# Performance work log

Measured on AMD Instinct MI355X. Metric: run time of the kernel, lower is better.

## Reference

```python
import jax, jax.numpy as jnp
import numpy as np

WINDOW_SIZE = 11
SIGMA = 1.5
LEVELS = 5
WEIGHTS = np.array([0.0448, 0.2856, 0.3001, 0.2363, 0.1333], dtype=np.float32)
C1 = 0.01 ** 2  # (0.01 * L)^2, L = 1
C2 = 0.03 ** 2


def _gauss_window(channel):
    x = np.arange(WINDOW_SIZE, dtype=np.float32) - WINDOW_SIZE // 2
    g = np.exp(-x ** 2 / (2.0 * SIGMA ** 2)).astype(np.float32)
    g = g / g.sum()
    w2 = np.outer(g, g)  # [ws, ws]
    w = np.broadcast_to(w2, (channel, 1, WINDOW_SIZE, WINDOW_SIZE)).copy()
    return jnp.asarray(w)


def _dwconv(x, w, channel):
    # depthwise conv, padding=0 (VALID), groups=channel
    return jax.lax.conv_general_dilated(
        x, w, window_strides=(1, 1), padding='VALID',
        dimension_numbers=('NCHW', 'OIHW', 'NCHW'),
        feature_group_count=channel)


def _ssim(img1, img2, window, channel):
    mu1 = _dwconv(img1, window, channel)
    mu2 = _dwconv(img2, window, channel)
    mu1_sq = mu1 * mu1
    mu2_sq = mu2 * mu2
    mu1_mu2 = mu1 * mu2
    sigma1_sq = _dwconv(img1 * img1, window, channel) - mu1_sq
    sigma2_sq = _dwconv(img2 * img2, window, channel) - mu2_sq
    sigma12 = _dwconv(img1 * img2, window, channel) - mu1_mu2
    v1 = 2.0 * sigma12 + C2
    v2 = sigma1_sq + sigma2_sq + C2
    cs = jnp.mean(v1 / v2)
    ssim_map = (2.0 * mu1_mu2 + C1) * v1 / ((mu1_sq + mu2_sq + C1) * v2)
    return jnp.mean(ssim_map), cs


def _avg_pool2(x):
    # avg_pool2d(kernel=2, stride=2), VALID
    s = jax.lax.reduce_window(x, 0.0, jax.lax.add, (1, 1, 2, 2), (1, 1, 2, 2), 'VALID')
    return s * 0.25


def setup_inputs() -> dict:
    key = jax.random.key(0)
    k1, k2 = jax.random.split(key)
    img1 = jax.random.uniform(k1, (16, 3, 512, 512), dtype=jnp.float32)
    img2 = jax.random.uniform(k2, (16, 3, 512, 512), dtype=jnp.float32)
    return {"img1": img1, "img2": img2}


def reference(img1, img2):
    channel = img1.shape[1]
    window = _gauss_window(channel)
    weights = jnp.asarray(WEIGHTS)
    mssim, mcs = [], []
    a, b = img1, img2
    for _ in range(LEVELS):  # fixed pyramid depth, shapes differ per level
        s, c = _ssim(a, b, window, channel)
        mssim.append(s)
        mcs.append(c)
        a = _avg_pool2(a)
        b = _avg_pool2(b)
    mssim = (jnp.stack(mssim) + 1.0) * 0.5  # normalize=True
    mcs = (jnp.stack(mcs) + 1.0) * 0.5
    return jnp.prod(mcs[:-1] ** weights[:-1]) * mssim[-1] ** weights[-1]
```

## Files before the change

### kernel.cpp

```cpp
#include <hip/hip_runtime.h>
#include <math.h>

#define WS 11
#define PAD 10
#define TW 32
#define TH 32
#define IH 42
#define NC 48
#define C1V 1.0e-4f
#define C2V 9.0e-4f

struct Params { float g[WS]; };
struct ROff { int off[5]; int cnt[5]; float inv[5]; };

template<int POOL>
__global__ __launch_bounds__(256, 6) void ssim_level_kernel(
    const float* __restrict__ img1, const float* __restrict__ img2,
    float* __restrict__ pool1, float* __restrict__ pool2,
    int H, int OH, int tilesX, Params P,
    float2* __restrict__ partial, int partial_off)
{
    __shared__ float4 rp[IH][TW];
    __shared__ float reds[4], redc[4];

    const int tid   = threadIdx.x;
    const int tileX = blockIdx.x % tilesX;
    const int tileY = blockIdx.x / tilesX;
    const int img   = blockIdx.y;
    const size_t ib = (size_t)img * H * H;
    const float* __restrict__ p1 = img1 + ib;
    const float* __restrict__ p2 = img2 + ib;
    const int ox0 = tileX * TW;
    const int oy0 = tileY * TH;

    for (int u = tid; u < IH * 8; u += 256) {
        const int r = u >> 3, cg = u & 7;
        const int y = min(oy0 + r, H - 1);
        const float* __restrict__ rowa = p1 + (size_t)y * H;
        const float* __restrict__ rowb = p2 + (size_t)y * H;
        float sv[16], dv[16];
#pragma unroll
        for (int q = 0; q < 4; ++q) {
            const int x = min(ox0 + cg * 4 + q * 4, H - 4);
            const float4 va = *(const float4*)(rowa + x);
            const float4 vb = *(const float4*)(rowb + x);
            sv[q*4+0] = va.x + vb.x;  dv[q*4+0] = va.x - vb.x;
            sv[q*4+1] = va.y + vb.y;  dv[q*4+1] = va.y - vb.y;
            sv[q*4+2] = va.z + vb.z;  dv[q*4+2] = va.z - vb.z;
            sv[q*4+3] = va.w + vb.w;  dv[q*4+3] = va.w - vb.w;
        }
        float m0[4] = {0,0,0,0}, m1[4] = {0,0,0,0};
        float m2[4] = {0,0,0,0}, m3[4] = {0,0,0,0};
#pragma unroll
        for (int i = 0; i < 14; ++i) {
            const float s = sv[i], d = dv[i];
            const float ss = s * s, dd = d * d;
#pragma unroll
            for (int j = 0; j < 4; ++j) {
                const int k = i - j;
                if (k >= 0 && k < WS) {
                    const float g = P.g[k];
                    m0[j] += g * s;  m1[j] += g * d;
                    m2[j] += g * ss; m3[j] += g * dd;
                }
            }
        }
        const int c0 = cg * 4, sw = r & 7;
#pragma unroll
        for (int j = 0; j < 4; ++j)
            rp[r][(c0 + j) ^ sw] = make_float4(m0[j], m1[j], m2[j], m3[j]);
    }
    __syncthreads();

    const int c  = tid & 31;
    const int r0 = (tid >> 5) * 4;
    float A0[4]={0,0,0,0}, A1[4]={0,0,0,0}, A2[4]={0,0,0,0}, A3[4]={0,0,0,0};
#pragma unroll
    for (int k = 0; k < 14; ++k) {
        const int R = r0 + k;
        const float4 v = rp[R][c ^ (R & 7)];
#pragma unroll
        for (int j = 0; j < 4; ++j) {
            const int t = k - j;
            if (t >= 0 && t < WS) {
                const float g = P.g[t];
                A0[j] += g * v.x; A1[j] += g * v.y;
                A2[j] += g * v.z; A3[j] += g * v.w;
            }
        }
    }
    float ssim_acc = 0.f, cs_acc = 0.f;
    const int ox = ox0 + c;
#pragma unroll
    for (int j = 0; j < 4; ++j) {
        const int oy = oy0 + r0 + j;
        if (oy < OH && ox < OH) {
            const float ms = A0[j], md = A1[j], Es = A2[j], Ed = A3[j];
            const float ms2 = ms * ms, md2 = md * md;
            const float mu12 = 0.25f * (ms2 - md2);
            const float musq = 0.5f  * (ms2 + md2);
            const float v1 = 0.5f * (Es - Ed) - 2.f * mu12 + C2V;
            const float v2 = 0.5f * (Es + Ed) - musq + C2V;
            const float rv2 = __builtin_amdgcn_rcpf(v2);
            const float cs  = v1 * rv2;
            const float ssim = (2.f * mu12 + C1V) *
                               __builtin_amdgcn_rcpf(musq + C1V) * cs;
            ssim_acc += ssim;
            cs_acc   += cs;
        }
    }

    if (POOL) {
        const int px = tid & 15, py = tid >> 4;
        const int yy = oy0 + 2 * py;
        const int xx = ox0 + 2 * px;
        const float2 a0 = *(const float2*)(p1 + (size_t)yy * H + xx);
        const float2 a1 = *(const float2*)(p1 + (size_t)(yy + 1) * H + xx);
        const float2 b0 = *(const float2*)(p2 + (size_t)yy * H + xx);
        const float2 b1 = *(const float2*)(p2 + (size_t)(yy + 1) * H + xx);
        const int h = H >> 1;
        const size_t ob = (size_t)img * h * h + (size_t)((oy0 >> 1) + py) * h + (ox0 >> 1) + px;
        pool1[ob] = 0.25f * (a0.x + a0.y + a1.x + a1.y);
        pool2[ob] = 0.25f * (b0.x + b0.y + b1.x + b1.y);
    }

#pragma unroll
    for (int off = 32; off > 0; off >>= 1) {
        ssim_acc += __shfl_down(ssim_acc, off);
        cs_acc   += __shfl_down(cs_acc, off);
    }
    const int wave = tid >> 6, lane = tid & 63;
    if (lane == 0) { reds[wave] = ssim_acc; redc[wave] = cs_acc; }
    __syncthreads();
    if (tid == 0) {
        const float s  = reds[0] + reds[1] + reds[2] + reds[3];
        const float cc = redc[0] + redc[1] + redc[2] + redc[3];
        partial[(size_t)partial_off + (size_t)blockIdx.y * gridDim.x + blockIdx.x] =
            make_float2(s, cc);
    }
}

__global__ __launch_bounds__(256) void reduce_final_kernel(
    const float2* __restrict__ partial, ROff ro, float* __restrict__ out)
{
    __shared__ float sS[5], sC[5];
    __shared__ float reds[4], redc[4];
    const int tid = threadIdx.x;
    for (int l = 0; l < 5; ++l) {
        float s = 0.f, c = 0.f;
        for (int i = tid; i < ro.cnt[l]; i += 256) {
            const float2 v = partial[ro.off[l] + i];
            s += v.x; c += v.y;
        }
#pragma unroll
        for (int off = 32; off > 0; off >>= 1) {
            s += __shfl_down(s, off);
            c += __shfl_down(c, off);
        }
        const int wave = tid >> 6, lane = tid & 63;
        if (lane == 0) { reds[wave] = s; redc[wave] = c; }
        __syncthreads();
        if (tid == 0) {
            sS[l] = (reds[0] + reds[1] + reds[2] + reds[3]) * ro.inv[l];
            sC[l] = (redc[0] + redc[1] + redc[2] + redc[3]) * ro.inv[l];
        }
        __syncthreads();
    }
    if (tid == 0) {
        const float w[5] = {0.0448f, 0.2856f, 0.3001f, 0.2363f, 0.1333f};
        float prod = 1.f;
#pragma unroll
        for (int i = 0; i < 4; ++i)
            prod *= powf((sC[i] + 1.f) * 0.5f, w[i]);
        prod *= powf((sS[4] + 1.f) * 0.5f, w[4]);
        out[0] = prod;
    }
}

extern "C" void kernel_launch(void* const* d_in, const int* in_sizes, int n_in,
                              void* d_out, int out_size, void* d_ws, size_t ws_size,
                              hipStream_t stream)
{
    const float* img1 = (const float*)d_in[0];
    const float* img2 = (const float*)d_in[1];
    float* out = (float*)d_out;
    float* ws  = (float*)d_ws;

    Params P;
    {
        double g[WS], sum = 0.0;
        for (int i = 0; i < WS; ++i) {
            double x = (double)i - (WS / 2);
            g[i] = exp(-x * x / (2.0 * 1.5 * 1.5));
            sum += g[i];
        }
        for (int i = 0; i < WS; ++i) P.g[i] = (float)(g[i] / sum);
    }

    float* p1[5]; float* p2[5];
    p1[0] = (float*)img1; p2[0] = (float*)img2;
    size_t o = 0;
    for (int l = 1; l < 5; ++l) {
        const int H = 512 >> l;
        p1[l] = ws + o; o += (size_t)NC * H * H;
        p2[l] = ws + o; o += (size_t)NC * H * H;
    }
    float2* partial = (float2*)(ws + o);
    (void)ws_size; (void)in_sizes; (void)n_in; (void)out_size;

    ROff ro;
    {
        int off = 0;
        for (int l = 0; l < 5; ++l) {
            const int H = 512 >> l, OH = H - PAD;
            const int tiles = (OH + TW - 1) / TW;
            ro.off[l] = off;
            ro.cnt[l] = tiles * tiles * NC;
            ro.inv[l] = 1.f / ((float)NC * OH * OH);
            off += ro.cnt[l];
        }
    }

    for (int l = 0; l < 5; ++l) {
        const int H = 512 >> l, OH = H - PAD;
        const int tiles = (OH + TW - 1) / TW;
        const dim3 grid(tiles * tiles, NC);
        if (l < 4)
            ssim_level_kernel<1><<<grid, 256, 0, stream>>>(
                p1[l], p2[l], p1[l + 1], p2[l + 1], H, OH, tiles, P, partial, ro.off[l]);
        else
            ssim_level_kernel<0><<<grid, 256, 0, stream>>>(
                p1[l], p2[l], nullptr, nullptr, H, OH, tiles, P, partial, ro.off[l]);
    }

    reduce_final_kernel<<<1, 256, 0, stream>>>(partial, ro, out);
}
```

Measured before the change: 119.7 us.

## Process vertical strips of tiles with a ring buffer to reuse halo rows

The per-tile SSIM kernel becomes a strip kernel. Each block walks CH vertically stacked 32x32 tiles and keeps the horizontal-convolution rows in a 64-row shared-memory ring buffer. The 10-row vertical halo is then computed once per strip rather than once per tile, which cuts redundant row-convolution work and global loads on the large levels. In exchange there are fewer blocks, serialized iterations with two barriers each, a lower launch-bounds occupancy hint, and an odd-stride padded layout in place of the XOR swizzle.

```diff
diff --git a/kernel.cpp b/kernel.cpp
--- a/kernel.cpp
+++ b/kernel.cpp
@@ -3,125 +3,143 @@
 
 #define WS 11
 #define PAD 10
-#define TW 32
-#define TH 32
-#define IH 42
 #define NC 48
 #define C1V 1.0e-4f
 #define C2V 9.0e-4f
+#define BROWS 64
+#define RST 33
 
 struct Params { float g[WS]; };
 struct ROff { int off[5]; int cnt[5]; float inv[5]; };
 
-template<int POOL>
-__global__ __launch_bounds__(256, 6) void ssim_level_kernel(
+__device__ __forceinline__ void row_conv_unit(
+    const float* __restrict__ rowa, const float* __restrict__ rowb,
+    const int xq[4], int cg, float4* __restrict__ rprow, const Params& P)
+{
+    float sv[16], dv[16];
+#pragma unroll
+    for (int q = 0; q < 4; ++q) {
+        const float4 va = *(const float4*)(rowa + xq[q]);
+        const float4 vb = *(const float4*)(rowb + xq[q]);
+        sv[q*4+0]=va.x+vb.x; dv[q*4+0]=va.x-vb.x;
+        sv[q*4+1]=va.y+vb.y; dv[q*4+1]=va.y-vb.y;
+        sv[q*4+2]=va.z+vb.z; dv[q*4+2]=va.z-vb.z;
+        sv[q*4+3]=va.w+vb.w; dv[q*4+3]=va.w-vb.w;
+    }
+    float m0[4]={0,0,0,0}, m1[4]={0,0,0,0}, m2[4]={0,0,0,0}, m3[4]={0,0,0,0};
+#pragma unroll
+    for (int i = 0; i < 14; ++i) {
+        const float s = sv[i], d = dv[i];
+        const float ss = s*s, dd = d*d;
+#pragma unroll
+        for (int j = 0; j < 4; ++j) {
+            const int k = i - j;
+            if (k >= 0 && k < WS) {
+                const float g = P.g[k];
+                m0[j]+=g*s; m1[j]+=g*d; m2[j]+=g*ss; m3[j]+=g*dd;
+            }
+        }
+    }
+#pragma unroll
+    for (int j = 0; j < 4; ++j)
+        rprow[cg*4 + j] = make_float4(m0[j], m1[j], m2[j], m3[j]);
+}
+
+template<int CH, int POOL>
+__global__ __launch_bounds__(256, 4) void ssim_strip_kernel(
     const float* __restrict__ img1, const float* __restrict__ img2,
     float* __restrict__ pool1, float* __restrict__ pool2,
     int H, int OH, int tilesX, Params P,
     float2* __restrict__ partial, int partial_off)
 {
-    __shared__ float4 rp[IH][TW];
+    __shared__ float4 rp[BROWS][RST];
     __shared__ float reds[4], redc[4];
-
     const int tid   = threadIdx.x;
     const int tileX = blockIdx.x % tilesX;
-    const int tileY = blockIdx.x / tilesX;
+    const int ty    = blockIdx.x / tilesX;
     const int img   = blockIdx.y;
     const size_t ib = (size_t)img * H * H;
     const float* __restrict__ p1 = img1 + ib;
     const float* __restrict__ p2 = img2 + ib;
-    const int ox0 = tileX * TW;
-    const int oy0 = tileY * TH;
-
-    for (int u = tid; u < IH * 8; u += 256) {
-        const int r = u >> 3, cg = u & 7;
-        const int y = min(oy0 + r, H - 1);
-        const float* __restrict__ rowa = p1 + (size_t)y * H;
-        const float* __restrict__ rowb = p2 + (size_t)y * H;
-        float sv[16], dv[16];
-#pragma unroll
-        for (int q = 0; q < 4; ++q) {
-            const int x = min(ox0 + cg * 4 + q * 4, H - 4);
-            const float4 va = *(const float4*)(rowa + x);
-            const float4 vb = *(const float4*)(rowb + x);
-            sv[q*4+0] = va.x + vb.x;  dv[q*4+0] = va.x - vb.x;
-            sv[q*4+1] = va.y + vb.y;  dv[q*4+1] = va.y - vb.y;
-            sv[q*4+2] = va.z + vb.z;  dv[q*4+2] = va.z - vb.z;
-            sv[q*4+3] = va.w + vb.w;  dv[q*4+3] = va.w - vb.w;
-        }
-        float m0[4] = {0,0,0,0}, m1[4] = {0,0,0,0};
-        float m2[4] = {0,0,0,0}, m3[4] = {0,0,0,0};
-#pragma unroll
-        for (int i = 0; i < 14; ++i) {
-            const float s = sv[i], d = dv[i];
-            const float ss = s * s, dd = d * d;
+    const int ox0 = tileX * 32;
+    const int oy0 = ty * (CH * 32);
+
+    const int r_unit = tid >> 3;
+    const int cg     = tid & 7;
+    int xq[4];
+#pragma unroll
+    for (int q = 0; q < 4; ++q) xq[q] = min(ox0 + cg*4 + q*4, H - 4);
+
+    const int cc  = tid & 31;
+    const int r0c = (tid >> 5) * 4;
+
+    if (tid < 80) {
+        const int Y = r_unit;
+        const int y = min(oy0 + Y, H - 1);
+        row_conv_unit(p1 + (size_t)y*H, p2 + (size_t)y*H, xq, cg,
+                      &rp[Y & (BROWS-1)][0], P);
+    }
+
+    float ssim_acc = 0.f, cs_acc = 0.f;
+
+    for (int t = 0; t < CH; ++t) {
+        {
+            const int Y = t*32 + 10 + r_unit;
+            const int y = min(oy0 + Y, H - 1);
+            row_conv_unit(p1 + (size_t)y*H, p2 + (size_t)y*H, xq, cg,
+                          &rp[Y & (BROWS-1)][0], P);
+        }
+        __syncthreads();
+
+        float A0[4]={0,0,0,0}, A1[4]={0,0,0,0}, A2[4]={0,0,0,0}, A3[4]={0,0,0,0};
+#pragma unroll
+        for (int k = 0; k < 14; ++k) {
+            const int Y = t*32 + r0c + k;
+            const float4 v = rp[Y & (BROWS-1)][cc];
 #pragma unroll
             for (int j = 0; j < 4; ++j) {
-                const int k = i - j;
-                if (k >= 0 && k < WS) {
-                    const float g = P.g[k];
-                    m0[j] += g * s;  m1[j] += g * d;
-                    m2[j] += g * ss; m3[j] += g * dd;
+                const int tt = k - j;
+                if (tt >= 0 && tt < WS) {
+                    const float g = P.g[tt];
+                    A0[j]+=g*v.x; A1[j]+=g*v.y; A2[j]+=g*v.z; A3[j]+=g*v.w;
                 }
             }
         }
-        const int c0 = cg * 4, sw = r & 7;
-#pragma unroll
-        for (int j = 0; j < 4; ++j)
-            rp[r][(c0 + j) ^ sw] = make_float4(m0[j], m1[j], m2[j], m3[j]);
-    }
-    __syncthreads();
-
-    const int c  = tid & 31;
-    const int r0 = (tid >> 5) * 4;
-    float A0[4]={0,0,0,0}, A1[4]={0,0,0,0}, A2[4]={0,0,0,0}, A3[4]={0,0,0,0};
-#pragma unroll
-    for (int k = 0; k < 14; ++k) {
-        const int R = r0 + k;
-        const float4 v = rp[R][c ^ (R & 7)];
+        const int ox = ox0 + cc;
 #pragma unroll
         for (int j = 0; j < 4; ++j) {
-            const int t = k - j;
-            if (t >= 0 && t < WS) {
-                const float g = P.g[t];
-                A0[j] += g * v.x; A1[j] += g * v.y;
-                A2[j] += g * v.z; A3[j] += g * v.w;
+            const int oy = oy0 + t*32 + r0c + j;
+            if (oy < OH && ox < OH) {
+                const float ms = A0[j], md = A1[j], Es = A2[j], Ed = A3[j];
+                const float ms2 = ms*ms, md2 = md*md;
+                const float mu12 = 0.25f * (ms2 - md2);
+                const float musq = 0.5f  * (ms2 + md2);
+                const float v1 = 0.5f * (Es - Ed) - 2.f*mu12 + C2V;
+                const float v2 = 0.5f * (Es + Ed) - musq + C2V;
+                const float rv2 = __builtin_amdgcn_rcpf(v2);
+                const float cs  = v1 * rv2;
+                const float ssim = (2.f*mu12 + C1V) *
+                                   __builtin_amdgcn_rcpf(musq + C1V) * cs;
+                ssim_acc += ssim;
+                cs_acc   += cs;
             }
         }
-    }
-    float ssim_acc = 0.f, cs_acc = 0.f;
-    const int ox = ox0 + c;
-#pragma unroll
-    for (int j = 0; j < 4; ++j) {
-        const int oy = oy0 + r0 + j;
-        if (oy < OH && ox < OH) {
-            const float ms = A0[j], md = A1[j], Es = A2[j], Ed = A3[j];
-            const float ms2 = ms * ms, md2 = md * md;
-            const float mu12 = 0.25f * (ms2 - md2);
-            const float musq = 0.5f  * (ms2 + md2);
-            const float v1 = 0.5f * (Es - Ed) - 2.f * mu12 + C2V;
-            const float v2 = 0.5f * (Es + Ed) - musq + C2V;
-            const float rv2 = __builtin_amdgcn_rcpf(v2);
-            const float cs  = v1 * rv2;
-            const float ssim = (2.f * mu12 + C1V) *
-                               __builtin_amdgcn_rcpf(musq + C1V) * cs;
-            ssim_acc += ssim;
-            cs_acc   += cs;
-        }
-    }
-
-    if (POOL) {
-        const int px = tid & 15, py = tid >> 4;
-        const int yy = oy0 + 2 * py;
-        const int xx = ox0 + 2 * px;
-        const float2 a0 = *(const float2*)(p1 + (size_t)yy * H + xx);
-        const float2 a1 = *(const float2*)(p1 + (size_t)(yy + 1) * H + xx);
-        const float2 b0 = *(const float2*)(p2 + (size_t)yy * H + xx);
-        const float2 b1 = *(const float2*)(p2 + (size_t)(yy + 1) * H + xx);
-        const int h = H >> 1;
-        const size_t ob = (size_t)img * h * h + (size_t)((oy0 >> 1) + py) * h + (ox0 >> 1) + px;
-        pool1[ob] = 0.25f * (a0.x + a0.y + a1.x + a1.y);
-        pool2[ob] = 0.25f * (b0.x + b0.y + b1.x + b1.y);
+
+        if (POOL) {
+            const int px = tid & 15, py = tid >> 4;
+            const int yy = oy0 + t*32 + 2*py;
+            const int xx = ox0 + 2*px;
+            const float2 a0 = *(const float2*)(p1 + (size_t)yy*H + xx);
+            const float2 a1 = *(const float2*)(p1 + (size_t)(yy+1)*H + xx);
+            const float2 b0 = *(const float2*)(p2 + (size_t)yy*H + xx);
+            const float2 b1 = *(const float2*)(p2 + (size_t)(yy+1)*H + xx);
+            const int h = H >> 1;
+            const size_t ob = (size_t)img*h*h +
+                              (size_t)(((oy0 + t*32) >> 1) + py)*h + (ox0 >> 1) + px;
+            pool1[ob] = 0.25f * (a0.x + a0.y + a1.x + a1.y);
+            pool2[ob] = 0.25f * (b0.x + b0.y + b1.x + b1.y);
+        }
+        __syncthreads();
     }
 
 #pragma unroll
@@ -134,9 +152,9 @@
     __syncthreads();
     if (tid == 0) {
         const float s  = reds[0] + reds[1] + reds[2] + reds[3];
-        const float cc = redc[0] + redc[1] + redc[2] + redc[3];
+        const float cc2 = redc[0] + redc[1] + redc[2] + redc[3];
         partial[(size_t)partial_off + (size_t)blockIdx.y * gridDim.x + blockIdx.x] =
-            make_float2(s, cc);
+            make_float2(s, cc2);
     }
 }
 
@@ -208,14 +226,16 @@
     float2* partial = (float2*)(ws + o);
     (void)ws_size; (void)in_sizes; (void)n_in; (void)out_size;
 
+    const int CHv[5] = {4, 2, 1, 1, 1};
     ROff ro;
     {
         int off = 0;
         for (int l = 0; l < 5; ++l) {
             const int H = 512 >> l, OH = H - PAD;
-            const int tiles = (OH + TW - 1) / TW;
+            const int tilesX = (OH + 31) / 32;
+            const int tilesY = (OH + CHv[l]*32 - 1) / (CHv[l]*32);
             ro.off[l] = off;
-            ro.cnt[l] = tiles * tiles * NC;
+            ro.cnt[l] = tilesX * tilesY * NC;
             ro.inv[l] = 1.f / ((float)NC * OH * OH);
             off += ro.cnt[l];
         }
@@ -223,14 +243,31 @@
 
     for (int l = 0; l < 5; ++l) {
         const int H = 512 >> l, OH = H - PAD;
-        const int tiles = (OH + TW - 1) / TW;
-        const dim3 grid(tiles * tiles, NC);
-        if (l < 4)
-            ssim_level_kernel<1><<<grid, 256, 0, stream>>>(
-                p1[l], p2[l], p1[l + 1], p2[l + 1], H, OH, tiles, P, partial, ro.off[l]);
-        else
-            ssim_level_kernel<0><<<grid, 256, 0, stream>>>(
-                p1[l], p2[l], nullptr, nullptr, H, OH, tiles, P, partial, ro.off[l]);
+        const int tilesX = (OH + 31) / 32;
+        const int tilesY = (OH + CHv[l]*32 - 1) / (CHv[l]*32);
+        const dim3 grid(tilesX * tilesY, NC);
+        switch (l) {
+        case 0:
+            ssim_strip_kernel<4,1><<<grid, 256, 0, stream>>>(
+                p1[0], p2[0], p1[1], p2[1], H, OH, tilesX, P, partial, ro.off[0]);
+            break;
+        case 1:
+            ssim_strip_kernel<2,1><<<grid, 256, 0, stream>>>(
+                p1[1], p2[1], p1[2], p2[2], H, OH, tilesX, P, partial, ro.off[1]);
+            break;
+        case 2:
+            ssim_strip_kernel<1,1><<<grid, 256, 0, stream>>>(
+                p1[2], p2[2], p1[3], p2[3], H, OH, tilesX, P, partial, ro.off[2]);
+            break;
+        case 3:
+            ssim_strip_kernel<1,1><<<grid, 256, 0, stream>>>(
+                p1[3], p2[3], p1[4], p2[4], H, OH, tilesX, P, partial, ro.off[3]);
+            break;
+        default:
+            ssim_strip_kernel<1,0><<<grid, 256, 0, stream>>>(
+                p1[4], p2[4], nullptr, nullptr, H, OH, tilesX, P, partial, ro.off[4]);
+            break;
+        }
     }
 
     reduce_final_kernel<<<1, 256, 0, stream>>>(partial, ro, out);
```

New measurement: 105.1 us. 12.2% less time.
